# Performance work log

Hardware: AMD Instinct MI355X
Metric: run time of the kernel (lower is better)

The kernel has to match this reference:

```python
import jax, jax.numpy as jnp
import numpy as np

B = 16384
NUM_INPUTS = 256
ACTION_DIM = 16
H0 = 1024
H1 = 1024
K = 128  # num_support
MIN_BIN_WIDTH = 0.001
MIN_BIN_HEIGHT = 0.001
MIN_DERIVATIVE = 0.001
EDGE_CONST = float(np.log(np.exp(1.0 - 0.001) - 1.0))  # log(exp(0.999)-1)
LN_EPS = 1e-5


def setup_inputs() -> dict:
    key = jax.random.key(0)
    ks = jax.random.split(key, 16)
    def lin(kw, kb, fan_out, fan_in):
        w = 1.0 / np.sqrt(fan_in)
        W = jax.random.uniform(kw, (fan_out, fan_in), jnp.float32, -w, w)
        b = jax.random.uniform(kb, (fan_out,), jnp.float32, -w, w)
        return W, b
    w1, b1 = lin(ks[0], ks[1], H0, NUM_INPUTS)
    w2, b2 = lin(ks[2], ks[3], H1, H0 + ACTION_DIM)
    wv, bv = lin(ks[4], ks[5], 3 * K - 1, H1)
    wa = jax.random.uniform(ks[6], (1, H1), jnp.float32, -0.003, 0.003)
    ba = jax.random.uniform(ks[7], (1,), jnp.float32, -0.0003, 0.0003)
    wb = jax.random.uniform(ks[8], (1, H1), jnp.float32, -0.003, 0.003)
    bb = jax.random.uniform(ks[9], (1,), jnp.float32, -0.0003, 0.0003)
    return {
        "inputs": jax.random.normal(ks[10], (B, NUM_INPUTS), jnp.float32),
        "actions": jax.random.normal(ks[11], (B, ACTION_DIM), jnp.float32),
        "w1": w1, "b1": b1,
        "ln1_g": jnp.ones((H0,), jnp.float32), "ln1_b": jnp.zeros((H0,), jnp.float32),
        "w2": w2, "b2": b2,
        "ln2_g": jnp.ones((H1,), jnp.float32), "ln2_b": jnp.zeros((H1,), jnp.float32),
        "wv": wv, "bv": bv,
        "wa": wa, "ba": ba,
        "wb": wb, "bb": bb,
    }


def _layernorm(x, g, b):
    mu = jnp.mean(x, axis=-1, keepdims=True)
    var = jnp.mean((x - mu) ** 2, axis=-1, keepdims=True)
    return (x - mu) / jnp.sqrt(var + LN_EPS) * g + b


def reference(inputs, actions, w1, b1, ln1_g, ln1_b, w2, b2, ln2_g, ln2_b,
              wv, bv, wa, ba, wb, bb):
    # trunk MLP
    x = jax.nn.relu(_layernorm(inputs @ w1.T + b1, ln1_g, ln1_b))
    x = jnp.concatenate([x, actions], axis=1)
    x = jax.nn.relu(_layernorm(x @ w2.T + b2, ln2_g, ln2_b))

    spline_param = x @ wv.T + bv            # [B, 3K-1]
    scale_a = jnp.exp(x @ wa.T + ba)        # [B, 1]
    scale_b = x @ wb.T + bb                 # [B, 1]

    W = spline_param[:, :K]
    H = spline_param[:, K:2 * K]
    Draw = spline_param[:, 2 * K:]          # [B, K-1]

    W = MIN_BIN_WIDTH + (1 - MIN_BIN_WIDTH * K) * jax.nn.softmax(W, axis=1)
    H = MIN_BIN_HEIGHT + (1 - MIN_BIN_HEIGHT * K) * jax.nn.softmax(H, axis=1)
    Dmid = MIN_DERIVATIVE + jax.nn.softplus(Draw)
    edge = jnp.full((W.shape[0], 1), EDGE_CONST, W.dtype)
    D = jnp.concatenate([edge, Dmid, edge], axis=-1)  # [B, K+1]

    zeros = jnp.zeros((W.shape[0], 1), W.dtype)
    cumwidths = jnp.concatenate([zeros, jnp.cumsum(W, axis=-1)], axis=-1)
    cumwidths = cumwidths.at[..., -1].set(1.0)        # [B, K+1]
    widths = cumwidths[..., 1:] - cumwidths[..., :-1]

    cumheights = jnp.concatenate([zeros, jnp.cumsum(H, axis=-1)], axis=-1)
    cumheights = scale_a * cumheights + scale_b       # [B, K+1]
    heights = cumheights[..., 1:] - cumheights[..., :-1]

    tau = (jnp.arange(K, dtype=W.dtype) + 0.5) / K    # [K]

    # brute-force searchsorted: sum(tau >= cumwidths) - 1
    bin_idx = jnp.sum(tau[None, :, None] >= cumwidths[:, None, :], axis=-1) - 1  # [B,K]

    gather = lambda t: jnp.take_along_axis(t, bin_idx, axis=-1)
    input_cumwidths = gather(cumwidths)
    input_bin_widths = gather(widths)
    input_cumheights = gather(cumheights)
    input_heights = gather(heights)
    delta = heights / widths
    input_delta = gather(delta)
    input_derivatives = gather(D)
    input_derivatives_plus_one = gather(D[..., 1:])

    theta = (tau[None, :] - input_cumwidths) / input_bin_widths
    theta_one_minus = theta * (1 - theta)
    numerator = input_heights * (input_delta * theta ** 2 + input_derivatives * theta_one_minus)
    denominator = input_delta + (input_derivatives + input_derivatives_plus_one - 2 * input_delta) * theta_one_minus
    return input_cumheights + numerator / denominator  # [B, K]
```

## Files before the change

kernel.cpp:

```cpp
#include <hip/hip_runtime.h>
#include <hip/hip_bf16.h>
#include <math.h>

#define BROWS      16384
#define LN_EPS_F   1e-5f
#define MINW       0.001f
#define MINH       0.001f
#define MIND       0.001f
#define EDGE_CONST_F 0.5397423505783211f

typedef __bf16 bf16x8 __attribute__((ext_vector_type(8)));
typedef float  f32x4  __attribute__((ext_vector_type(4)));

__device__ __forceinline__ ushort f2bf(float x) {
    union { float f; unsigned u; } v; v.f = x;
    unsigned u = v.u;
    u += 0x7fffu + ((u >> 16) & 1u);
    return (ushort)(u >> 16);
}
__device__ __forceinline__ float bf2f(ushort h) {
    union { unsigned u; float f; } v; v.u = ((unsigned)h) << 16;
    return v.f;
}

__global__ __launch_bounds__(256, 2)
void gemm_bf16x3(const ushort* __restrict__ Ah, const ushort* __restrict__ Al,
                 const ushort* __restrict__ Bh, const ushort* __restrict__ Bl,
                 const float* __restrict__ bias,
                 float* __restrict__ C, int ldc, int Nstore, int Kpad)
{
    __shared__ ushort lds[32768];
    const int tid  = threadIdx.x;
    const int wid  = tid >> 6;
    const int lane = tid & 63;
    const int bm0  = blockIdx.x * 128;
    const int bn0  = blockIdx.y * 128;
    const int wm   = wid >> 1;
    const int wn   = wid & 1;
    const int l15  = lane & 15;
    const int kg   = lane >> 4;

    const ushort* gsrc[8];
    {
        const ushort* pb[4] = {Ah, Al, Bh, Bl};
        #pragma unroll
        for (int i = 0; i < 8; ++i) {
            const int F     = i * 4096 + tid * 16;
            const int pl    = F >> 13;
            const int chunk = (F & 8191) >> 4;
            const int kgrp  = chunk >> 7;
            const int row   = chunk & 127;
            const int r0    = (pl < 2) ? bm0 : bn0;
            gsrc[i] = pb[pl] + (size_t)(r0 + row) * Kpad + kgrp * 8;
        }
    }
    #define STAGE_ONE(i, bufbase, kelem)                                       \
        __builtin_amdgcn_global_load_lds(                                      \
            (const __attribute__((address_space(1))) void*)(gsrc[i] + (kelem)),\
            (__attribute__((address_space(3))) void*)(&lds[(bufbase) + (i) * 2048 + wid * 512]), \
            16, 0, 0)

    f32x4 acc[4][4];
    #pragma unroll
    for (int m = 0; m < 4; ++m)
        #pragma unroll
        for (int n = 0; n < 4; ++n)
            acc[m][n] = (f32x4){0.f, 0.f, 0.f, 0.f};

    const int aoff = kg * 1024 + (wm * 64 + l15) * 8;
    const int boff = 8192 + kg * 1024 + (wn * 64 + l15) * 8;
    const int nt = Kpad >> 5;

    STAGE_ONE(0, 0, 0); STAGE_ONE(1, 0, 0); STAGE_ONE(2, 0, 0); STAGE_ONE(3, 0, 0);
    STAGE_ONE(4, 0, 0); STAGE_ONE(5, 0, 0); STAGE_ONE(6, 0, 0); STAGE_ONE(7, 0, 0);
    int cur = 0;

    for (int t = 0; t < nt; ++t) {
        const int nxt = cur ^ 1;
        const int nb  = nxt * 16384;
        const int cb  = cur * 16384;
        const int ke  = (t + 1) * 32;
        const bool pf = (t + 1 < nt);

        if (pf) { STAGE_ONE(0, nb, ke); STAGE_ONE(1, nb, ke); STAGE_ONE(2, nb, ke); }
        if (pf) { asm volatile("s_waitcnt vmcnt(3)" ::: "memory"); }
        else    { asm volatile("s_waitcnt vmcnt(0)" ::: "memory"); }
        __builtin_amdgcn_sched_barrier(0);
        __builtin_amdgcn_s_barrier();
        asm volatile("" ::: "memory");

        bf16x8 aH[4], aL[4], bH[4], bL[4];
        #pragma unroll
        for (int m = 0; m < 4; ++m) aH[m] = *(const bf16x8*)&lds[cb + aoff + m * 128];
        #pragma unroll
        for (int n = 0; n < 4; ++n) bH[n] = *(const bf16x8*)&lds[cb + boff + n * 128];
        asm volatile("s_waitcnt lgkmcnt(0)" ::: "memory");
        __builtin_amdgcn_sched_barrier(0);
        __builtin_amdgcn_s_setprio(1);
        #pragma unroll
        for (int m = 0; m < 4; ++m)
            #pragma unroll
            for (int n = 0; n < 4; ++n)
                acc[m][n] = __builtin_amdgcn_mfma_f32_16x16x32_bf16(aH[m], bH[n], acc[m][n], 0, 0, 0);
        __builtin_amdgcn_s_setprio(0);
        __builtin_amdgcn_s_barrier();
        asm volatile("" ::: "memory");

        if (pf) { STAGE_ONE(3, nb, ke); STAGE_ONE(4, nb, ke); STAGE_ONE(5, nb, ke); }
        #pragma unroll
        for (int n = 0; n < 4; ++n) bL[n] = *(const bf16x8*)&lds[cb + 4096 + boff + n * 128];
        asm volatile("s_waitcnt lgkmcnt(0)" ::: "memory");
        __builtin_amdgcn_sched_barrier(0);
        __builtin_amdgcn_s_setprio(1);
        #pragma unroll
        for (int m = 0; m < 4; ++m)
            #pragma unroll
            for (int n = 0; n < 4; ++n)
                acc[m][n] = __builtin_amdgcn_mfma_f32_16x16x32_bf16(aH[m], bL[n], acc[m][n], 0, 0, 0);
        __builtin_amdgcn_s_setprio(0);
        __builtin_amdgcn_s_barrier();
        asm volatile("" ::: "memory");

        if (pf) { STAGE_ONE(6, nb, ke); STAGE_ONE(7, nb, ke); }
        #pragma unroll
        for (int m = 0; m < 4; ++m) aL[m] = *(const bf16x8*)&lds[cb + 4096 + aoff + m * 128];
        asm volatile("s_waitcnt lgkmcnt(0)" ::: "memory");
        __builtin_amdgcn_sched_barrier(0);
        __builtin_amdgcn_s_setprio(1);
        #pragma unroll
        for (int m = 0; m < 4; ++m)
            #pragma unroll
            for (int n = 0; n < 4; ++n)
                acc[m][n] = __builtin_amdgcn_mfma_f32_16x16x32_bf16(aL[m], bH[n], acc[m][n], 0, 0, 0);
        __builtin_amdgcn_s_setprio(0);
        __builtin_amdgcn_s_barrier();
        asm volatile("" ::: "memory");
        cur = nxt;
    }
    #undef STAGE_ONE

    #pragma unroll
    for (int n = 0; n < 4; ++n) {
        const int col = bn0 + wn * 64 + n * 16 + l15;
        if (col < Nstore) {
            const float bs = bias[col];
            #pragma unroll
            for (int m = 0; m < 4; ++m) {
                const int row = bm0 + wm * 64 + m * 16 + kg * 4;
                #pragma unroll
                for (int r = 0; r < 4; ++r)
                    C[(size_t)(row + r) * ldc + col] = acc[m][n][r] + bs;
            }
        }
    }
}

__global__ __launch_bounds__(256)
void ln_relu_split(const float* __restrict__ Y,
                   const float* __restrict__ g, const float* __restrict__ b,
                   ushort* __restrict__ Xh, ushort* __restrict__ Xl, int xstride,
                   const float* __restrict__ actions, int dopad)
{
    __shared__ float red[4];
    const int row = blockIdx.x;
    const int tid = threadIdx.x;
    const float* y = Y + (size_t)row * 1024;

    const float4 v = *(const float4*)(y + tid * 4);
    float s = v.x + v.y + v.z + v.w;
    #pragma unroll
    for (int off = 32; off > 0; off >>= 1) s += __shfl_down(s, off, 64);
    if ((tid & 63) == 0) red[tid >> 6] = s;
    __syncthreads();
    const float mu = (red[0] + red[1] + red[2] + red[3]) * (1.f / 1024.f);
    __syncthreads();
    const float d0 = v.x - mu, d1 = v.y - mu, d2 = v.z - mu, d3 = v.w - mu;
    float s2 = d0 * d0 + d1 * d1 + d2 * d2 + d3 * d3;
    #pragma unroll
    for (int off = 32; off > 0; off >>= 1) s2 += __shfl_down(s2, off, 64);
    if ((tid & 63) == 0) red[tid >> 6] = s2;
    __syncthreads();
    const float var = (red[0] + red[1] + red[2] + red[3]) * (1.f / 1024.f);
    const float inv = 1.0f / sqrtf(var + LN_EPS_F);

    float o0 = fmaxf(0.f, d0 * inv * g[tid * 4 + 0] + b[tid * 4 + 0]);
    float o1 = fmaxf(0.f, d1 * inv * g[tid * 4 + 1] + b[tid * 4 + 1]);
    float o2 = fmaxf(0.f, d2 * inv * g[tid * 4 + 2] + b[tid * 4 + 2]);
    float o3 = fmaxf(0.f, d3 * inv * g[tid * 4 + 3] + b[tid * 4 + 3]);

    ushort4 oh, ol;
    oh.x = f2bf(o0); ol.x = f2bf(o0 - bf2f(oh.x));
    oh.y = f2bf(o1); ol.y = f2bf(o1 - bf2f(oh.y));
    oh.z = f2bf(o2); ol.z = f2bf(o2 - bf2f(oh.z));
    oh.w = f2bf(o3); ol.w = f2bf(o3 - bf2f(oh.w));
    *(ushort4*)(Xh + (size_t)row * xstride + tid * 4) = oh;
    *(ushort4*)(Xl + (size_t)row * xstride + tid * 4) = ol;

    if (actions != nullptr && tid < 16) {
        const float a = actions[(size_t)row * 16 + tid];
        const ushort h = f2bf(a);
        Xh[(size_t)row * xstride + 1024 + tid] = h;
        Xl[(size_t)row * xstride + 1024 + tid] = f2bf(a - bf2f(h));
    }
    if (dopad && tid >= 16 && tid < 64) {
        Xh[(size_t)row * xstride + 1024 + tid] = 0;
        Xl[(size_t)row * xstride + 1024 + tid] = 0;
    }
}

__global__ __launch_bounds__(256)
void split_mat(const float* __restrict__ src, int scols,
               ushort* __restrict__ Dh, ushort* __restrict__ Dl,
               int dcols, int total)
{
    const int idx = (blockIdx.x * 256 + threadIdx.x) * 4;
    if (idx >= total) return;
    const int r = idx / dcols, c = idx % dcols;
    float e[4];
    if (c + 3 < scols) {
        const float4 v = *(const float4*)(src + (size_t)r * scols + c);
        e[0] = v.x; e[1] = v.y; e[2] = v.z; e[3] = v.w;
    } else {
        #pragma unroll
        for (int j = 0; j < 4; ++j)
            e[j] = (c + j < scols) ? src[(size_t)r * scols + c + j] : 0.f;
    }
    ushort4 h, l;
    h.x = f2bf(e[0]); l.x = f2bf(e[0] - bf2f(h.x));
    h.y = f2bf(e[1]); l.y = f2bf(e[1] - bf2f(h.y));
    h.z = f2bf(e[2]); l.z = f2bf(e[2] - bf2f(h.z));
    h.w = f2bf(e[3]); l.w = f2bf(e[3] - bf2f(h.w));
    *(ushort4*)(Dh + idx) = h;
    *(ushort4*)(Dl + idx) = l;
}

__global__ __launch_bounds__(256)
void build_wcat_split(const float* __restrict__ wv, const float* __restrict__ wa,
                      const float* __restrict__ wb, const float* __restrict__ bv,
                      const float* __restrict__ ba, const float* __restrict__ bb,
                      ushort* __restrict__ Wh, ushort* __restrict__ Wl,
                      float* __restrict__ bcat)
{
    const int idx = blockIdx.x * 256 + threadIdx.x;
    if (idx < 512 * 1024) {
        const int n = idx >> 10, k = idx & 1023;
        const float v = (n < 383) ? wv[n * 1024 + k]
                       : (n == 383) ? wa[k]
                       : (n == 384) ? wb[k] : 0.f;
        const ushort h = f2bf(v);
        Wh[idx] = h;
        Wl[idx] = f2bf(v - bf2f(h));
    }
    if (idx < 512) {
        bcat[idx] = (idx < 383) ? bv[idx] : (idx == 383) ? ba[0]
                   : (idx == 384) ? bb[0] : 0.f;
    }
}

__device__ __forceinline__ float softplus_f(float x) {
    return (x > 20.f) ? x : log1pf(expf(x));
}

__global__ __launch_bounds__(256)
void spline_rq(const float* __restrict__ P, float* __restrict__ Out)
{
    __shared__ float cw[4][132];
    __shared__ float ch[4][132];
    __shared__ float Dv[4][132];
    const int wid  = threadIdx.x >> 6;
    const int lane = threadIdx.x & 63;
    const int r    = blockIdx.x * 4 + wid;
    const float* p = P + (size_t)r * 385;
    const int e0 = 2 * lane, e1 = 2 * lane + 1;

    const float sa = expf(p[383]);
    const float sb = p[384];

    const float w0 = p[e0], w1 = p[e1];
    float mx = fmaxf(w0, w1);
    #pragma unroll
    for (int off = 1; off < 64; off <<= 1) mx = fmaxf(mx, __shfl_xor(mx, off, 64));
    const float xw0 = expf(w0 - mx), xw1 = expf(w1 - mx);
    float sw = xw0 + xw1;
    #pragma unroll
    for (int off = 1; off < 64; off <<= 1) sw += __shfl_xor(sw, off, 64);
    const float cwn = (1.f - MINW * 128.f) / sw;
    const float Wv0 = MINW + cwn * xw0;
    const float Wv1 = MINW + cwn * xw1;
    float s = Wv0 + Wv1;
    #pragma unroll
    for (int off = 1; off < 64; off <<= 1) {
        const float t = __shfl_up(s, off, 64);
        if (lane >= off) s += t;
    }
    if (lane == 0) cw[wid][0] = 0.f;
    cw[wid][e1]     = s - Wv1;
    cw[wid][e1 + 1] = (lane == 63) ? 1.0f : s;

    const float h0 = p[128 + e0], h1 = p[128 + e1];
    float mh = fmaxf(h0, h1);
    #pragma unroll
    for (int off = 1; off < 64; off <<= 1) mh = fmaxf(mh, __shfl_xor(mh, off, 64));
    const float xh0 = expf(h0 - mh), xh1 = expf(h1 - mh);
    float sh = xh0 + xh1;
    #pragma unroll
    for (int off = 1; off < 64; off <<= 1) sh += __shfl_xor(sh, off, 64);
    const float chn = (1.f - MINH * 128.f) / sh;
    const float Hv0 = MINH + chn * xh0;
    const float Hv1 = MINH + chn * xh1;
    float t2 = Hv0 + Hv1;
    #pragma unroll
    for (int off = 1; off < 64; off <<= 1) {
        const float t = __shfl_up(t2, off, 64);
        if (lane >= off) t2 += t;
    }
    if (lane == 0) ch[wid][0] = sb;
    ch[wid][e1]     = sa * (t2 - Hv1) + sb;
    ch[wid][e1 + 1] = sa * t2 + sb;

    if (lane == 0) { Dv[wid][0] = EDGE_CONST_F; Dv[wid][128] = EDGE_CONST_F; }
    Dv[wid][e0 + 1] = MIND + softplus_f(p[256 + e0]);
    if (lane < 63) Dv[wid][e1 + 1] = MIND + softplus_f(p[256 + e1]);

    __syncthreads();

    #pragma unroll
    for (int t = 0; t < 2; ++t) {
        const int e = 2 * lane + t;
        const float tau = ((float)e + 0.5f) * (1.f / 128.f);
        int lo = 0, hi = 128;
        #pragma unroll
        for (int it = 0; it < 7; ++it) {
            const int mid = (lo + hi) >> 1;
            if (cw[wid][mid] <= tau) lo = mid; else hi = mid;
        }
        const int bin = lo;
        const float icw = cw[wid][bin];
        const float ibw = cw[wid][bin + 1] - icw;
        const float ich = ch[wid][bin];
        const float ih  = ch[wid][bin + 1] - ich;
        const float idelta = ih / ibw;
        const float dd0 = Dv[wid][bin];
        const float dd1 = Dv[wid][bin + 1];
        const float theta = (tau - icw) / ibw;
        const float tom = theta * (1.f - theta);
        const float num = ih * (idelta * theta * theta + dd0 * tom);
        const float den = idelta + (dd0 + dd1 - 2.f * idelta) * tom;
        Out[(size_t)r * 128 + e] = ich + num / den;
    }
}

extern "C" void kernel_launch(void* const* d_in, const int* in_sizes, int n_in,
                              void* d_out, int out_size, void* d_ws, size_t ws_size,
                              hipStream_t stream) {
    const float* inputs  = (const float*)d_in[0];
    const float* actions = (const float*)d_in[1];
    const float* w1      = (const float*)d_in[2];
    const float* b1      = (const float*)d_in[3];
    const float* ln1_g   = (const float*)d_in[4];
    const float* ln1_b   = (const float*)d_in[5];
    const float* w2      = (const float*)d_in[6];
    const float* b2      = (const float*)d_in[7];
    const float* ln2_g   = (const float*)d_in[8];
    const float* ln2_b   = (const float*)d_in[9];
    const float* wv      = (const float*)d_in[10];
    const float* bv      = (const float*)d_in[11];
    const float* wa      = (const float*)d_in[12];
    const float* ba      = (const float*)d_in[13];
    const float* wb      = (const float*)d_in[14];
    const float* bb      = (const float*)d_in[15];

    float*  ws_y  = (float*)d_ws;
    ushort* ws_Xh = (ushort*)(ws_y + (size_t)16384 * 1024);
    ushort* ws_Xl = ws_Xh + (size_t)16384 * 1088;
    ushort* w1h   = ws_Xl + (size_t)16384 * 1088;
    ushort* w1l   = w1h + 1024 * 256;
    ushort* w2h   = w1l + 1024 * 256;
    ushort* w2l   = w2h + 1024 * 1088;
    ushort* wch   = w2l + 1024 * 1088;
    ushort* wcl   = wch + 512 * 1024;
    float*  bcat  = (float*)(wcl + 512 * 1024);

    split_mat<<<(16384 * 256 / 4 + 255) / 256, 256, 0, stream>>>(inputs, 256, ws_Xh, ws_Xl, 256, 16384 * 256);
    split_mat<<<(1024 * 256 / 4 + 255) / 256, 256, 0, stream>>>(w1, 256, w1h, w1l, 256, 1024 * 256);
    split_mat<<<(1024 * 1088 / 4 + 255) / 256, 256, 0, stream>>>(w2, 1040, w2h, w2l, 1088, 1024 * 1088);
    build_wcat_split<<<(512 * 1024 + 255) / 256, 256, 0, stream>>>(wv, wa, wb, bv, ba, bb, wch, wcl, bcat);

    gemm_bf16x3<<<dim3(128, 8), 256, 0, stream>>>(ws_Xh, ws_Xl, w1h, w1l, b1, ws_y, 1024, 1024, 256);
    ln_relu_split<<<16384, 256, 0, stream>>>(ws_y, ln1_g, ln1_b, ws_Xh, ws_Xl, 1088, actions, 1);

    gemm_bf16x3<<<dim3(128, 8), 256, 0, stream>>>(ws_Xh, ws_Xl, w2h, w2l, b2, ws_y, 1024, 1024, 1088);
    ln_relu_split<<<16384, 256, 0, stream>>>(ws_y, ln2_g, ln2_b, ws_Xh, ws_Xl, 1024, nullptr, 0);

    gemm_bf16x3<<<dim3(128, 4), 256, 0, stream>>>(ws_Xh, ws_Xl, wch, wcl, bcat, ws_y, 385, 385, 1024);

    spline_rq<<<4096, 256, 0, stream>>>(ws_y, (float*)d_out);
}
```

Before: 433.1 us.

## Use 8-wave 256x256 GEMM tiles with finer-grained prefetch pipelining

```diff
diff --git a/kernel.cpp b/kernel.cpp
--- a/kernel.cpp
+++ b/kernel.cpp
@@ -23,121 +23,138 @@
     return v.f;
 }
 
-__global__ __launch_bounds__(256, 2)
-void gemm_bf16x3(const ushort* __restrict__ Ah, const ushort* __restrict__ Al,
-                 const ushort* __restrict__ Bh, const ushort* __restrict__ Bl,
-                 const float* __restrict__ bias,
-                 float* __restrict__ C, int ldc, int Nstore, int Kpad)
+#define WAITV(n) do { asm volatile("s_waitcnt vmcnt(" #n ")" ::: "memory"); \
+                      __builtin_amdgcn_sched_barrier(0); } while (0)
+#define BARF()   do { __builtin_amdgcn_s_barrier(); \
+                      asm volatile("" ::: "memory"); } while (0)
+
+template<int MREP>
+__global__ __launch_bounds__(512, 2)
+void gemm_bf16x3_8p(const ushort* __restrict__ Ah, const ushort* __restrict__ Al,
+                    const ushort* __restrict__ Bh, const ushort* __restrict__ Bl,
+                    const float* __restrict__ bias,
+                    float* __restrict__ C, int ldc, int Nstore, int Kpad)
 {
-    __shared__ ushort lds[32768];
+    constexpr int BM   = MREP * 32;
+    constexpr int LA   = MREP / 4;
+    constexpr int AH0  = 0;
+    constexpr int AL0  = BM * 32;
+    constexpr int BH0  = 2 * BM * 32;
+    constexpr int BL0  = 2 * BM * 32 + 8192;
+    constexpr int SBUF = 2 * BM * 32 + 16384;
+
+    __shared__ ushort lds[2 * SBUF];
+
     const int tid  = threadIdx.x;
     const int wid  = tid >> 6;
     const int lane = tid & 63;
-    const int bm0  = blockIdx.x * 128;
-    const int bn0  = blockIdx.y * 128;
-    const int wm   = wid >> 1;
-    const int wn   = wid & 1;
+    const int wm   = wid >> 2;
+    const int wn   = wid & 3;
     const int l15  = lane & 15;
     const int kg   = lane >> 4;
-
-    const ushort* gsrc[8];
-    {
-        const ushort* pb[4] = {Ah, Al, Bh, Bl};
-        #pragma unroll
-        for (int i = 0; i < 8; ++i) {
-            const int F     = i * 4096 + tid * 16;
-            const int pl    = F >> 13;
-            const int chunk = (F & 8191) >> 4;
-            const int kgrp  = chunk >> 7;
-            const int row   = chunk & 127;
-            const int r0    = (pl < 2) ? bm0 : bn0;
-            gsrc[i] = pb[pl] + (size_t)(r0 + row) * Kpad + kgrp * 8;
+    const int bm0  = blockIdx.x * BM;
+    const int bn0  = blockIdx.y * 256;
+
+    const ushort* sP[4][2];
+    #pragma unroll
+    for (int i = 0; i < 2; ++i) {
+        if (i < LA) {
+            const int c    = i * 512 + tid;
+            const int kgrp = c / BM;
+            const int row  = c % BM;
+            const size_t off = (size_t)(bm0 + row) * Kpad + kgrp * 8;
+            sP[0][i] = Ah + off;
+            sP[1][i] = Al + off;
         }
-    }
-    #define STAGE_ONE(i, bufbase, kelem)                                       \
-        __builtin_amdgcn_global_load_lds(                                      \
-            (const __attribute__((address_space(1))) void*)(gsrc[i] + (kelem)),\
-            (__attribute__((address_space(3))) void*)(&lds[(bufbase) + (i) * 2048 + wid * 512]), \
-            16, 0, 0)
-
-    f32x4 acc[4][4];
-    #pragma unroll
-    for (int m = 0; m < 4; ++m)
+        {
+            const int c    = i * 512 + tid;
+            const int kgrp = c >> 8;
+            const int row  = c & 255;
+            const size_t off = (size_t)(bn0 + row) * Kpad + kgrp * 8;
+            sP[2][i] = Bh + off;
+            sP[3][i] = Bl + off;
+        }
+    }
+    auto STAGE = [&](int pi, int dbase, int cnt, int bb, int ke) {
+        #pragma unroll
+        for (int i = 0; i < 2; ++i)
+            if (i < cnt)
+                __builtin_amdgcn_global_load_lds(
+                    (const __attribute__((address_space(1))) void*)(sP[pi][i] + ke),
+                    (__attribute__((address_space(3))) void*)(&lds[bb + dbase + i * 4096 + wid * 512]),
+                    16, 0, 0);
+    };
+
+    f32x4 acc[MREP][4];
+    #pragma unroll
+    for (int m = 0; m < MREP; ++m)
         #pragma unroll
         for (int n = 0; n < 4; ++n)
             acc[m][n] = (f32x4){0.f, 0.f, 0.f, 0.f};
 
-    const int aoff = kg * 1024 + (wm * 64 + l15) * 8;
-    const int boff = 8192 + kg * 1024 + (wn * 64 + l15) * 8;
+    const int arow = (wm * (BM / 2) + l15) * 8;
+    const int brow = (wn * 64 + l15) * 8;
     const int nt = Kpad >> 5;
 
-    STAGE_ONE(0, 0, 0); STAGE_ONE(1, 0, 0); STAGE_ONE(2, 0, 0); STAGE_ONE(3, 0, 0);
-    STAGE_ONE(4, 0, 0); STAGE_ONE(5, 0, 0); STAGE_ONE(6, 0, 0); STAGE_ONE(7, 0, 0);
-    int cur = 0;
+    STAGE(0, AH0, LA, 0, 0); STAGE(2, BH0, 2, 0, 0);
+    STAGE(3, BL0, 2, 0, 0);  STAGE(1, AL0, LA, 0, 0);
+    if constexpr (MREP == 8) WAITV(4); else WAITV(3);
+    BARF();
 
     for (int t = 0; t < nt; ++t) {
-        const int nxt = cur ^ 1;
-        const int nb  = nxt * 16384;
-        const int cb  = cur * 16384;
-        const int ke  = (t + 1) * 32;
+        const int cb = (t & 1) * SBUF;
+        const int nb = ((t + 1) & 1) * SBUF;
+        const int ke = (t + 1) * 32;
         const bool pf = (t + 1 < nt);
 
-        if (pf) { STAGE_ONE(0, nb, ke); STAGE_ONE(1, nb, ke); STAGE_ONE(2, nb, ke); }
-        if (pf) { asm volatile("s_waitcnt vmcnt(3)" ::: "memory"); }
-        else    { asm volatile("s_waitcnt vmcnt(0)" ::: "memory"); }
-        __builtin_amdgcn_sched_barrier(0);
-        __builtin_amdgcn_s_barrier();
-        asm volatile("" ::: "memory");
-
-        bf16x8 aH[4], aL[4], bH[4], bL[4];
-        #pragma unroll
-        for (int m = 0; m < 4; ++m) aH[m] = *(const bf16x8*)&lds[cb + aoff + m * 128];
-        #pragma unroll
-        for (int n = 0; n < 4; ++n) bH[n] = *(const bf16x8*)&lds[cb + boff + n * 128];
-        asm volatile("s_waitcnt lgkmcnt(0)" ::: "memory");
-        __builtin_amdgcn_sched_barrier(0);
+        bf16x8 aH[MREP], bH[4], bL[4], aL[MREP];
+        #pragma unroll
+        for (int m = 0; m < MREP; ++m)
+            aH[m] = *(const bf16x8*)&lds[cb + AH0 + kg * (BM * 8) + arow + m * 128];
+        #pragma unroll
+        for (int n = 0; n < 4; ++n)
+            bH[n] = *(const bf16x8*)&lds[cb + BH0 + kg * 2048 + brow + n * 128];
+        if (pf) { STAGE(0, AH0, LA, nb, ke); STAGE(2, BH0, 2, nb, ke); }
         __builtin_amdgcn_s_setprio(1);
         #pragma unroll
-        for (int m = 0; m < 4; ++m)
+        for (int m = 0; m < MREP; ++m)
             #pragma unroll
             for (int n = 0; n < 4; ++n)
                 acc[m][n] = __builtin_amdgcn_mfma_f32_16x16x32_bf16(aH[m], bH[n], acc[m][n], 0, 0, 0);
         __builtin_amdgcn_s_setprio(0);
-        __builtin_amdgcn_s_barrier();
-        asm volatile("" ::: "memory");
-
-        if (pf) { STAGE_ONE(3, nb, ke); STAGE_ONE(4, nb, ke); STAGE_ONE(5, nb, ke); }
-        #pragma unroll
-        for (int n = 0; n < 4; ++n) bL[n] = *(const bf16x8*)&lds[cb + 4096 + boff + n * 128];
-        asm volatile("s_waitcnt lgkmcnt(0)" ::: "memory");
-        __builtin_amdgcn_sched_barrier(0);
+        if (pf) { if constexpr (MREP == 8) WAITV(6); else WAITV(4); }
+        else    { if constexpr (MREP == 8) WAITV(2); else WAITV(1); }
+        BARF();
+
+        #pragma unroll
+        for (int n = 0; n < 4; ++n)
+            bL[n] = *(const bf16x8*)&lds[cb + BL0 + kg * 2048 + brow + n * 128];
+        if (pf) STAGE(3, BL0, 2, nb, ke);
         __builtin_amdgcn_s_setprio(1);
         #pragma unroll
-        for (int m = 0; m < 4; ++m)
+        for (int m = 0; m < MREP; ++m)
             #pragma unroll
             for (int n = 0; n < 4; ++n)
                 acc[m][n] = __builtin_amdgcn_mfma_f32_16x16x32_bf16(aH[m], bL[n], acc[m][n], 0, 0, 0);
         __builtin_amdgcn_s_setprio(0);
-        __builtin_amdgcn_s_barrier();
-        asm volatile("" ::: "memory");
-
-        if (pf) { STAGE_ONE(6, nb, ke); STAGE_ONE(7, nb, ke); }
-        #pragma unroll
-        for (int m = 0; m < 4; ++m) aL[m] = *(const bf16x8*)&lds[cb + 4096 + aoff + m * 128];
-        asm volatile("s_waitcnt lgkmcnt(0)" ::: "memory");
-        __builtin_amdgcn_sched_barrier(0);
+        if (pf) { if constexpr (MREP == 8) WAITV(6); else WAITV(5); }
+        else    WAITV(0);
+        BARF();
+
+        #pragma unroll
+        for (int m = 0; m < MREP; ++m)
+            aL[m] = *(const bf16x8*)&lds[cb + AL0 + kg * (BM * 8) + arow + m * 128];
+        if (pf) STAGE(1, AL0, LA, nb, ke);
         __builtin_amdgcn_s_setprio(1);
         #pragma unroll
-        for (int m = 0; m < 4; ++m)
+        for (int m = 0; m < MREP; ++m)
             #pragma unroll
             for (int n = 0; n < 4; ++n)
                 acc[m][n] = __builtin_amdgcn_mfma_f32_16x16x32_bf16(aL[m], bH[n], acc[m][n], 0, 0, 0);
         __builtin_amdgcn_s_setprio(0);
-        __builtin_amdgcn_s_barrier();
-        asm volatile("" ::: "memory");
-        cur = nxt;
-    }
-    #undef STAGE_ONE
+        if (pf) { if constexpr (MREP == 8) WAITV(4); else WAITV(3); }
+        BARF();
+    }
 
     #pragma unroll
     for (int n = 0; n < 4; ++n) {
@@ -145,8 +162,8 @@
         if (col < Nstore) {
             const float bs = bias[col];
             #pragma unroll
-            for (int m = 0; m < 4; ++m) {
-                const int row = bm0 + wm * 64 + m * 16 + kg * 4;
+            for (int m = 0; m < MREP; ++m) {
+                const int row = bm0 + wm * (BM / 2) + m * 16 + kg * 4;
                 #pragma unroll
                 for (int r = 0; r < 4; ++r)
                     C[(size_t)(row + r) * ldc + col] = acc[m][n][r] + bs;
@@ -386,13 +403,13 @@
     split_mat<<<(1024 * 1088 / 4 + 255) / 256, 256, 0, stream>>>(w2, 1040, w2h, w2l, 1088, 1024 * 1088);
     build_wcat_split<<<(512 * 1024 + 255) / 256, 256, 0, stream>>>(wv, wa, wb, bv, ba, bb, wch, wcl, bcat);
 
-    gemm_bf16x3<<<dim3(128, 8), 256, 0, stream>>>(ws_Xh, ws_Xl, w1h, w1l, b1, ws_y, 1024, 1024, 256);
+    gemm_bf16x3_8p<8><<<dim3(64, 4), 512, 0, stream>>>(ws_Xh, ws_Xl, w1h, w1l, b1, ws_y, 1024, 1024, 256);
     ln_relu_split<<<16384, 256, 0, stream>>>(ws_y, ln1_g, ln1_b, ws_Xh, ws_Xl, 1088, actions, 1);
 
-    gemm_bf16x3<<<dim3(128, 8), 256, 0, stream>>>(ws_Xh, ws_Xl, w2h, w2l, b2, ws_y, 1024, 1024, 1088);
+    gemm_bf16x3_8p<8><<<dim3(64, 4), 512, 0, stream>>>(ws_Xh, ws_Xl, w2h, w2l, b2, ws_y, 1024, 1024, 1088);
     ln_relu_split<<<16384, 256, 0, stream>>>(ws_y, ln2_g, ln2_b, ws_Xh, ws_Xl, 1024, nullptr, 0);
 
-    gemm_bf16x3<<<dim3(128, 4), 256, 0, stream>>>(ws_Xh, ws_Xl, wch, wcl, bcat, ws_y, 385, 385, 1024);
+    gemm_bf16x3_8p<4><<<dim3(128, 2), 512, 0, stream>>>(ws_Xh, ws_Xl, wch, wcl, bcat, ws_y, 385, 385, 1024);
 
     spline_rq<<<4096, 256, 0, stream>>>(ws_y, (float*)d_out);
 }
```

After: 421.4 us. 1.03x faster.
